# Kernel tuning notes

Measured on AMD Instinct MI355X. Metric: run time of the kernel, lower is better.

Reference implementation:

```python
import jax, jax.numpy as jnp
import numpy as np

S = 4096          # num tokens
H = 2304          # hidden_size
NQ = 8            # num query heads
NKV = 4           # num kv heads
HD = 256          # head_dim
INTER = 9216      # intermediate_size
SOFTCAP = 50.0    # attn_logit_softcapping
WINDOW = 1024     # sliding window
EPS = 1e-6
THETA = 10000.0
SCALE = 256.0 ** -0.5  # query_pre_attn_scalar ** -0.5


def rmsnorm(x, w, eps=EPS):
    # GemmaRMSNorm: x / rms(x) * (1 + w)
    var = jnp.mean(x * x, axis=-1, keepdims=True)
    return x * jax.lax.rsqrt(var + eps) * (1.0 + w)


def apply_rope(x, positions):
    # x: [S, nh, HD], neox style (rotate halves)
    half = HD // 2
    inv_freq = 1.0 / (THETA ** (jnp.arange(0, half, dtype=jnp.float32) / half))
    freqs = positions.astype(jnp.float32)[:, None] * inv_freq[None, :]  # [S, half]
    cos = jnp.cos(freqs)[:, None, :]
    sin = jnp.sin(freqs)[:, None, :]
    x1, x2 = x[..., :half], x[..., half:]
    return jnp.concatenate([x1 * cos - x2 * sin, x2 * cos + x1 * sin], axis=-1)


def setup_inputs() -> dict:
    key = jax.random.key(0)
    ks = jax.random.split(key, 6)
    w_std = 0.02
    return {
        "positions": jnp.arange(S, dtype=jnp.int32),
        "hidden_states": jax.random.normal(ks[0], (S, H), dtype=jnp.float32),
        "w_qkv": jax.random.normal(ks[1], (H, (NQ + 2 * NKV) * HD), dtype=jnp.float32) * w_std,
        "w_o": jax.random.normal(ks[2], (NQ * HD, H), dtype=jnp.float32) * w_std,
        "w_gate_up": jax.random.normal(ks[3], (H, 2 * INTER), dtype=jnp.float32) * w_std,
        "w_down": jax.random.normal(ks[4], (INTER, H), dtype=jnp.float32) * w_std,
        "w_in_ln": jnp.zeros((H,), jnp.float32),
        "w_post_attn_ln": jnp.zeros((H,), jnp.float32),
        "w_pre_ff_ln": jnp.zeros((H,), jnp.float32),
        "w_post_ff_ln": jnp.zeros((H,), jnp.float32),
    }


def attention(positions, h, w_qkv, w_o):
    qkv = h @ w_qkv  # [S, (NQ+2*NKV)*HD]
    q, k, v = jnp.split(qkv, [NQ * HD, (NQ + NKV) * HD], axis=-1)
    q = q.reshape(S, NQ, HD)
    k = k.reshape(S, NKV, HD)
    v = v.reshape(S, NKV, HD)
    q = apply_rope(q, positions)
    k = apply_rope(k, positions)
    # GQA: repeat kv heads
    rep = NQ // NKV
    k = jnp.repeat(k, rep, axis=1)  # [S, NQ, HD]
    v = jnp.repeat(v, rep, axis=1)
    scores = jnp.einsum("qhd,khd->hqk", q, k) * SCALE  # [NQ, S, S]
    # Gemma2 logit soft-capping
    scores = SOFTCAP * jnp.tanh(scores / SOFTCAP)
    # causal + sliding window mask
    i = jnp.arange(S)[:, None]
    j = jnp.arange(S)[None, :]
    ok = (j <= i) & (i - j < WINDOW)
    scores = jnp.where(ok[None], scores, -jnp.inf)
    probs = jax.nn.softmax(scores, axis=-1)
    out = jnp.einsum("hqk,khd->qhd", probs, v).reshape(S, NQ * HD)
    return out @ w_o


def mlp(x, w_gate_up, w_down):
    gu = x @ w_gate_up  # [S, 2*INTER]
    gate, up = jnp.split(gu, 2, axis=-1)
    return (jax.nn.gelu(gate, approximate=True) * up) @ w_down


def reference(positions, hidden_states, w_qkv, w_o, w_gate_up, w_down,
              w_in_ln, w_post_attn_ln, w_pre_ff_ln, w_post_ff_ln):
    # residual is None on entry (first layer semantics)
    residual = hidden_states
    h = rmsnorm(hidden_states, w_in_ln)
    h = attention(positions, h, w_qkv, w_o)
    h = rmsnorm(h, w_post_attn_ln)
    # fused add + norm: residual <- h + residual ; h <- norm(residual)
    residual = h + residual
    h = rmsnorm(residual, w_pre_ff_ln)
    h = mlp(h, w_gate_up, w_down)
    h = rmsnorm(h, w_post_ff_ln)
    return (h, residual)
```

## Files before the change

### kernel.cpp

```cpp
#include <hip/hip_runtime.h>
#include <cstdint>
#include <cmath>

#define S_LEN 4096
#define H_DIM 2304
#define NQH   8
#define NKVH  4
#define HDIM  256
#define INTER 9216
#define QKV_N 4096
#define QH    2048
#define KVH   1024

typedef __attribute__((ext_vector_type(4))) float  f32x4;
typedef __attribute__((ext_vector_type(8))) __bf16 bf16x8;

__device__ __forceinline__ __bf16 f2bf(float f) {
  union { float f; unsigned u; } x; x.f = f;
  unsigned r = (x.u + 0x7fffu + ((x.u >> 16) & 1u)) >> 16;
  union { unsigned short s; __bf16 b; } y; y.s = (unsigned short)r;
  return y.b;
}

__device__ __forceinline__ void g2l16(const void* g, void* l) {
  __builtin_amdgcn_global_load_lds(
      (__attribute__((address_space(1))) void*)(uintptr_t)g,
      (__attribute__((address_space(3))) void*)(uint32_t)(uintptr_t)l, 16, 0, 0);
}

__device__ __forceinline__ float block_sum(float v, float* sbuf) {
  #pragma unroll
  for (int o = 32; o > 0; o >>= 1) v += __shfl_xor(v, o);
  __syncthreads();
  if ((threadIdx.x & 63) == 0) sbuf[threadIdx.x >> 6] = v;
  __syncthreads();
  return sbuf[0] + sbuf[1] + sbuf[2] + sbuf[3];
}

__global__ void conv_t64(const float* __restrict__ src, __bf16* __restrict__ dst,
                         int srcStride, int dstStride) {
  __shared__ float t[64 * 65];
  int tid = threadIdx.x;
  long n0 = (long)blockIdx.x * 64, k0 = (long)blockIdx.y * 64;
  int tx = tid & 15;
  int ky = tid >> 4;
  #pragma unroll
  for (int l = 0; l < 4; ++l) {
    int k = ky + l * 16;
    f32x4 v = *(const f32x4*)(src + (k0 + k) * srcStride + n0 + tx * 4);
    #pragma unroll
    for (int e = 0; e < 4; ++e) t[(tx * 4 + e) * 65 + k] = v[e];
  }
  __syncthreads();
  int ny = tid >> 2, kc = (tid & 3) * 16;
  bf16x8 a, b;
  #pragma unroll
  for (int i = 0; i < 8; ++i) a[i] = f2bf(t[ny * 65 + kc + i]);
  #pragma unroll
  for (int i = 0; i < 8; ++i) b[i] = f2bf(t[ny * 65 + kc + 8 + i]);
  __bf16* d = dst + (n0 + ny) * dstStride + k0 + kc;
  *(bf16x8*)d = a;
  *(bf16x8*)(d + 8) = b;
}

__device__ __forceinline__ int gu_map(int n) {
  int t = n >> 7, w = (n >> 6) & 1, j = (n >> 4) & 3, c = n & 15;
  int a = t * 64 + w * 32 + ((j >> 1) << 4) + c;
  return (j & 1) ? (INTER + a) : a;
}

__global__ void conv_gu64(const float* __restrict__ src, __bf16* __restrict__ dst) {
  __shared__ float t[64 * 65];
  int tid = threadIdx.x;
  long n0 = (long)blockIdx.x * 64, k0 = (long)blockIdx.y * 64;
  int tx = tid & 15, ky = tid >> 4;
  int sc = gu_map((int)n0 + tx * 4);
  #pragma unroll
  for (int l = 0; l < 4; ++l) {
    int k = ky + l * 16;
    f32x4 v = *(const f32x4*)(src + (k0 + k) * (2 * INTER) + sc);
    #pragma unroll
    for (int e = 0; e < 4; ++e) t[(tx * 4 + e) * 65 + k] = v[e];
  }
  __syncthreads();
  int ny = tid >> 2, kc = (tid & 3) * 16;
  bf16x8 a, b;
  #pragma unroll
  for (int i = 0; i < 8; ++i) a[i] = f2bf(t[ny * 65 + kc + i]);
  #pragma unroll
  for (int i = 0; i < 8; ++i) b[i] = f2bf(t[ny * 65 + kc + 8 + i]);
  __bf16* d = dst + (n0 + ny) * H_DIM + k0 + kc;
  *(bf16x8*)d = a;
  *(bf16x8*)(d + 8) = b;
}

__global__ void rms_in_kernel(const float* __restrict__ x, const float* __restrict__ w,
                              __bf16* __restrict__ out) {
  __shared__ float sbuf[4];
  int row = blockIdx.x, tid = threadIdx.x;
  const float* xr = x + (long)row * H_DIM;
  float v[9]; float ss = 0.f;
  #pragma unroll
  for (int i = 0; i < 9; ++i) { v[i] = xr[tid + i * 256]; ss += v[i] * v[i]; }
  ss = block_sum(ss, sbuf);
  float inv = rsqrtf(ss * (1.0f / H_DIM) + 1e-6f);
  #pragma unroll
  for (int i = 0; i < 9; ++i)
    out[(long)row * H_DIM + tid + i * 256] = f2bf(v[i] * inv * (1.f + w[tid + i * 256]));
}

__global__ void rms_post_attn_kernel(const float* __restrict__ P, const float* __restrict__ hidden,
                                     const float* __restrict__ w_post, const float* __restrict__ w_pre,
                                     float* __restrict__ resid, __bf16* __restrict__ x2) {
  __shared__ float sbuf[4];
  int row = blockIdx.x, tid = threadIdx.x;
  const float* pr = P + (long)row * H_DIM;
  const float* hr = hidden + (long)row * H_DIM;
  float pv[9]; float ss = 0.f;
  #pragma unroll
  for (int i = 0; i < 9; ++i) { pv[i] = pr[tid + i * 256]; ss += pv[i] * pv[i]; }
  ss = block_sum(ss, sbuf);
  float inv = rsqrtf(ss * (1.0f / H_DIM) + 1e-6f);
  float rv[9]; float ss2 = 0.f;
  #pragma unroll
  for (int i = 0; i < 9; ++i) {
    int c = tid + i * 256;
    float hn = pv[i] * inv * (1.f + w_post[c]);
    rv[i] = hn + hr[c];
    resid[(long)row * H_DIM + c] = rv[i];
    ss2 += rv[i] * rv[i];
  }
  ss2 = block_sum(ss2, sbuf);
  float inv2 = rsqrtf(ss2 * (1.0f / H_DIM) + 1e-6f);
  #pragma unroll
  for (int i = 0; i < 9; ++i) {
    int c = tid + i * 256;
    x2[(long)row * H_DIM + c] = f2bf(rv[i] * inv2 * (1.f + w_pre[c]));
  }
}

__global__ void rms_final_kernel(const float* __restrict__ x, const float* __restrict__ w,
                                 float* __restrict__ out) {
  __shared__ float sbuf[4];
  int row = blockIdx.x, tid = threadIdx.x;
  const float* xr = x + (long)row * H_DIM;
  float v[9]; float ss = 0.f;
  #pragma unroll
  for (int i = 0; i < 9; ++i) { v[i] = xr[tid + i * 256]; ss += v[i] * v[i]; }
  ss = block_sum(ss, sbuf);
  float inv = rsqrtf(ss * (1.0f / H_DIM) + 1e-6f);
  #pragma unroll
  for (int i = 0; i < 9; ++i)
    out[(long)row * H_DIM + tid + i * 256] = v[i] * inv * (1.f + w[tid + i * 256]);
}

__global__ void rope_kernel(const float* __restrict__ qkv, const int* __restrict__ positions,
                            __bf16* __restrict__ Qr, __bf16* __restrict__ Kr) {
  int row = blockIdx.x, tid = threadIdx.x;
  float pos = (float)positions[row];
  const float LOG_TH_128 = 9.210340371976184f / 128.f;
  bool isQ = tid < 128;
  int c = isQ ? tid : (tid - 128);
  int hh = c >> 4;
  int d0 = (c & 15) * 8;
  const float* base = qkv + (long)row * QKV_N + (isQ ? 0 : QH) + hh * 256;
  f32x4 x1a = *(const f32x4*)(base + d0);
  f32x4 x1b = *(const f32x4*)(base + d0 + 4);
  f32x4 x2a = *(const f32x4*)(base + d0 + 128);
  f32x4 x2b = *(const f32x4*)(base + d0 + 132);
  bf16x8 lo, hi;
  #pragma unroll
  for (int j = 0; j < 8; ++j) {
    float x1 = j < 4 ? x1a[j] : x1b[j - 4];
    float x2 = j < 4 ? x2a[j] : x2b[j - 4];
    float fr = pos * expf(-(float)(d0 + j) * LOG_TH_128);
    float sn, cs; sincosf(fr, &sn, &cs);
    lo[j] = f2bf(x1 * cs - x2 * sn);
    hi[j] = f2bf(x2 * cs + x1 * sn);
  }
  __bf16* out = (isQ ? Qr + (long)row * QH : Kr + (long)row * KVH) + hh * 256;
  *(bf16x8*)(out + d0) = lo;
  *(bf16x8*)(out + 128 + d0) = hi;
}

template <int EPI>
__global__ void gemm_bt(const __bf16* __restrict__ A, const __bf16* __restrict__ B,
                        void* __restrict__ Cout, int K, int ldc) {
  __shared__ __bf16 As[128 * 64];
  __shared__ __bf16 Bs[128 * 64];
  int tid = threadIdx.x;
  int wave = tid >> 6, lane = tid & 63;
  int wm = wave >> 1, wn = wave & 1;
  int q4 = lane >> 4, l15 = lane & 15;

  int nwgx = gridDim.x;
  int nwg = nwgx * gridDim.y;
  int orig = blockIdx.y * nwgx + blockIdx.x;
  int qd = nwg >> 3, rm = nwg & 7;
  int xcd = orig & 7, idx = orig >> 3;
  int swz = (xcd < rm ? xcd * (qd + 1) : rm * (qd + 1) + (xcd - rm) * qd) + idx;
  long bm = (long)(swz / nwgx) * 128, bn = (long)(swz % nwgx) * 128;

  int r8 = tid >> 3;
  int cs = (tid & 7) ^ (r8 & 7);
  const __bf16* Ag = A + (bm + r8) * K + cs * 8;
  const __bf16* Bg = B + (bn + r8) * K + cs * 8;
  __bf16* Asd = As + tid * 8;
  __bf16* Bsd = Bs + tid * 8;

  int moff[4], noff[4];
  #pragma unroll
  for (int i = 0; i < 4; ++i) {
    moff[i] = (wm * 64 + i * 16 + l15) * 64;
    noff[i] = (wn * 64 + i * 16 + l15) * 64;
  }
  int c0 = (q4 ^ (l15 & 7)) * 8;
  f32x4 acc[4][4] = {};

  for (int k0 = 0; k0 < K; k0 += 64) {
    #pragma unroll
    for (int l = 0; l < 4; ++l) {
      g2l16(Ag + (long)(l * 32) * K, Asd + l * 2048);
      g2l16(Bg + (long)(l * 32) * K, Bsd + l * 2048);
    }
    Ag += 64; Bg += 64;
    __syncthreads();
    #pragma unroll
    for (int ks = 0; ks < 2; ++ks) {
      int cc = c0 ^ (ks * 32);
      bf16x8 af[4], bfv[4];
      #pragma unroll
      for (int i = 0; i < 4; ++i) af[i]  = *(const bf16x8*)(As + moff[i] + cc);
      #pragma unroll
      for (int j = 0; j < 4; ++j) bfv[j] = *(const bf16x8*)(Bs + noff[j] + cc);
      #pragma unroll
      for (int i = 0; i < 4; ++i)
        #pragma unroll
        for (int j = 0; j < 4; ++j)
          acc[i][j] = __builtin_amdgcn_mfma_f32_16x16x32_bf16(af[i], bfv[j], acc[i][j], 0, 0, 0);
    }
    __syncthreads();
  }

  if (EPI == 0) {
    float* C = (float*)Cout;
    #pragma unroll
    for (int i = 0; i < 4; ++i)
      #pragma unroll
      for (int r = 0; r < 4; ++r) {
        long m = bm + wm * 64 + i * 16 + q4 * 4 + r;
        #pragma unroll
        for (int j = 0; j < 4; ++j)
          C[m * ldc + bn + wn * 64 + j * 16 + l15] = acc[i][j][r];
      }
  } else {
    __bf16* C = (__bf16*)Cout;
    #pragma unroll
    for (int i = 0; i < 4; ++i)
      #pragma unroll
      for (int r = 0; r < 4; ++r) {
        long m = bm + wm * 64 + i * 16 + q4 * 4 + r;
        #pragma unroll
        for (int jj = 0; jj < 2; ++jj) {
          float gt = acc[i][2 * jj][r];
          float up = acc[i][2 * jj + 1][r];
          float u = 0.7978845608f * (gt + 0.044715f * gt * gt * gt);
          float e = __builtin_amdgcn_exp2f(u * 2.8853900817779268f);
          float gl = gt * (1.0f - __builtin_amdgcn_rcpf(e + 1.0f));
          long a = (bn >> 1) + wn * 32 + jj * 16 + l15;
          C[m * ldc + a] = f2bf(gl * up);
        }
      }
  }
}

template <int EPI>
__global__ __launch_bounds__(512, 2)
void gemm8(const __bf16* __restrict__ A, const __bf16* __restrict__ B,
           void* __restrict__ Cout, int K, int ldc) {
  __shared__ __bf16 As[2][16384];
  __shared__ __bf16 Bs[2][16384];
  const __bf16* Asb = (const __bf16*)As;
  const __bf16* Bsb = (const __bf16*)Bs;

  int tid = threadIdx.x;
  int wave = tid >> 6, lane = tid & 63;
  int wm = wave >> 2;
  int wn = wave & 3;
  int q4 = lane >> 4, l15 = lane & 15;
  int xk = l15 & 7;

  int nwgx = gridDim.x;
  int nwg = nwgx * gridDim.y;
  int orig = blockIdx.y * nwgx + blockIdx.x;
  int qd = nwg >> 3, rm = nwg & 7;
  int xcd = orig & 7, idx = orig >> 3;
  int swz = (xcd < rm ? xcd * (qd + 1) : rm * (qd + 1) + (xcd - rm) * qd) + idx;
  long bm = (long)(swz / nwgx) * 256;
  long bn = (long)(swz % nwgx) * 256;

  int rr = tid >> 3;
  int cs = (tid & 7) ^ (rr & 7);
  const __bf16* Ag = A + (bm + rr) * (long)K + cs * 8;
  const __bf16* Bg = B + (bn + rr) * (long)K + cs * 8;
  __bf16* Asd = (__bf16*)As + tid * 8;
  __bf16* Bsd = (__bf16*)Bs + tid * 8;

#define ST_A(buf, h, kof) do { \
    g2l16(Ag + ((h) * 128LL      ) * K + (kof), Asd + (buf) * 16384 + (h) * 8192); \
    g2l16(Ag + ((h) * 128LL + 64 ) * K + (kof), Asd + (buf) * 16384 + (h) * 8192 + 4096); } while (0)
#define ST_B(buf, h, kof) do { \
    g2l16(Bg + ((h) * 128LL      ) * K + (kof), Bsd + (buf) * 16384 + (h) * 8192); \
    g2l16(Bg + ((h) * 128LL + 64 ) * K + (kof), Bsd + (buf) * 16384 + (h) * 8192 + 4096); } while (0)

  int aOff[4], bOff[4];
  #pragma unroll
  for (int i = 0; i < 4; ++i) {
    aOff[i] = (wm * 64 + i * 16 + l15) * 64;
    bOff[i] = (wn * 64 + i * 16 + l15) * 64;
  }

#define PH_LOAD_A(buf, mh, ks) \
  { _Pragma("unroll") for (int f = 0; f < 4; ++f) \
      afr[f] = *(const bf16x8*)(Asb + (buf) * 16384 + (mh) * 8192 + aOff[f] + ((((ks) * 4 + q4) ^ xk) * 8)); }
#define PH_LOAD_B(buf) \
  { _Pragma("unroll") for (int ks2 = 0; ks2 < 2; ++ks2) \
    _Pragma("unroll") for (int j = 0; j < 4; ++j) \
      bfr[ks2][j] = *(const bf16x8*)(Bsb + (buf) * 16384 + bOff[j] + (((ks2 * 4 + q4) ^ xk) * 8)); }
#define PH_CORE(mh, ks) \
  __builtin_amdgcn_s_barrier(); \
  asm volatile("s_waitcnt lgkmcnt(0)" ::: "memory"); \
  __builtin_amdgcn_s_setprio(1); \
  { _Pragma("unroll") for (int f = 0; f < 4; ++f) \
    _Pragma("unroll") for (int j = 0; j < 4; ++j) \
      acc[(mh) * 4 + f][j] = __builtin_amdgcn_mfma_f32_16x16x32_bf16(afr[f], bfr[ks][j], acc[(mh) * 4 + f][j], 0, 0, 0); } \
  __builtin_amdgcn_s_setprio(0)
#define BAR   __builtin_amdgcn_s_barrier()
#define WVM6  asm volatile("s_waitcnt vmcnt(6)" ::: "memory")
#define WVM0  asm volatile("s_waitcnt vmcnt(0)" ::: "memory")

  f32x4 acc[8][4] = {};
  bf16x8 bfr[2][4];
  bf16x8 afr[4];

  int nt = K >> 6;
  int nit = (nt >> 1) - 1;

  ST_B(0, 0, 0); ST_B(0, 1, 0); ST_A(0, 0, 0); ST_A(0, 1, 0);
  ST_B(1, 0, 64); ST_B(1, 1, 64); ST_A(1, 0, 64);
  WVM6;
  BAR;

  for (int it = 0; it < nit; ++it) {
    const long k0 = (long)it * 128;
    PH_LOAD_B(0); PH_LOAD_A(0, 0, 0); ST_A(1, 1, k0 + 64);
    asm volatile("s_waitcnt lgkmcnt(8)" ::: "memory");
    PH_CORE(0, 0); BAR;
    PH_LOAD_A(0, 0, 1); ST_B(0, 0, k0 + 128);
    PH_CORE(0, 1); BAR;
    PH_LOAD_A(0, 1, 0); ST_B(0, 1, k0 + 128);
    PH_CORE(1, 0); BAR;
    PH_LOAD_A(0, 1, 1); ST_A(0, 0, k0 + 128);
    PH_CORE(1, 1); WVM6; BAR;
    PH_LOAD_B(1); PH_LOAD_A(1, 0, 0); ST_A(0, 1, k0 + 128);
    asm volatile("s_waitcnt lgkmcnt(8)" ::: "memory");
    PH_CORE(0, 0); BAR;
    PH_LOAD_A(1, 0, 1); ST_B(1, 0, k0 + 192);
    PH_CORE(0, 1); BAR;
    PH_LOAD_A(1, 1, 0); ST_B(1, 1, k0 + 192);
    PH_CORE(1, 0); BAR;
    PH_LOAD_A(1, 1, 1); ST_A(1, 0, k0 + 192);
    PH_CORE(1, 1); WVM6; BAR;
  }

  {
    const long k0 = (long)(nt - 2) * 64;
    PH_LOAD_B(0); PH_LOAD_A(0, 0, 0); ST_A(1, 1, k0 + 64);
    asm volatile("s_waitcnt lgkmcnt(8)" ::: "memory");
    PH_CORE(0, 0); BAR;
    PH_LOAD_A(0, 0, 1); PH_CORE(0, 1); BAR;
    PH_LOAD_A(0, 1, 0); PH_CORE(1, 0); BAR;
    PH_LOAD_A(0, 1, 1); PH_CORE(1, 1); WVM0; BAR;
    PH_LOAD_B(1); PH_LOAD_A(1, 0, 0); PH_CORE(0, 0); BAR;
    PH_LOAD_A(1, 0, 1); PH_CORE(0, 1); BAR;
    PH_LOAD_A(1, 1, 0); PH_CORE(1, 0); BAR;
    PH_LOAD_A(1, 1, 1); PH_CORE(1, 1);
  }

#undef ST_A
#undef ST_B
#undef PH_LOAD_A
#undef PH_LOAD_B
#undef PH_CORE
#undef BAR
#undef WVM6
#undef WVM0

  if (EPI == 0) {
    float* C = (float*)Cout;
    #pragma unroll
    for (int mi = 0; mi < 8; ++mi) {
      int mh = mi >> 2, f = mi & 3;
      #pragma unroll
      for (int r = 0; r < 4; ++r) {
        long m = bm + mh * 128 + wm * 64 + f * 16 + q4 * 4 + r;
        #pragma unroll
        for (int j = 0; j < 4; ++j)
          C[m * ldc + bn + wn * 64 + j * 16 + l15] = acc[mi][j][r];
      }
    }
  } else {
    __bf16* C = (__bf16*)Cout;
    #pragma unroll
    for (int mi = 0; mi < 8; ++mi) {
      int mh = mi >> 2, f = mi & 3;
      #pragma unroll
      for (int r = 0; r < 4; ++r) {
        long m = bm + mh * 128 + wm * 64 + f * 16 + q4 * 4 + r;
        #pragma unroll
        for (int jj = 0; jj < 2; ++jj) {
          float gt = acc[mi][2 * jj][r];
          float up = acc[mi][2 * jj + 1][r];
          float u = 0.7978845608f * (gt + 0.044715f * gt * gt * gt);
          float e = __builtin_amdgcn_exp2f(u * 2.8853900817779268f);
          float gl = gt * (1.0f - __builtin_amdgcn_rcpf(e + 1.0f));
          long a = (bn >> 1) + (wn >> 1) * 64 + (wn & 1) * 32 + jj * 16 + l15;
          C[m * ldc + a] = f2bf(gl * up);
        }
      }
    }
  }
}

__global__ void attn_kernel(const __bf16* __restrict__ Qr, const __bf16* __restrict__ Kr,
                            const __bf16* __restrict__ VT, __bf16* __restrict__ AT) {
  __shared__ __bf16 Kt[64 * 256];
  __shared__ __bf16 Vt[256 * 64];
  __shared__ __bf16 Pt[4][16 * 72];
  int tid = threadIdx.x, wave = tid >> 6, lane = tid & 63;
  int q4 = lane >> 4, l15 = lane & 15;
  int h = blockIdx.y, hk = h >> 1;
  int qb = blockIdx.x * 64;
  int wqb = qb + wave * 16;

  bf16x8 qf[8];
  {
    const __bf16* qp = Qr + (long)(wqb + l15) * QH + h * HDIM + q4 * 8;
    #pragma unroll
    for (int ks = 0; ks < 8; ++ks) qf[ks] = *(const bf16x8*)(qp + ks * 32);
  }
  f32x4 Oa[16] = {};
  float lsum[4] = {0.f, 0.f, 0.f, 0.f};

  int csk = (tid & 31) ^ ((tid >> 5) & 7);
  const __bf16* Kh = Kr + (long)(tid >> 5) * KVH + hk * HDIM + csk * 8;
  int csv = (tid & 7) ^ ((tid >> 3) & 7);
  const __bf16* Vh = VT + (long)(hk * HDIM + (tid >> 3)) * S_LEN + csv * 8;

  int lo = qb - 1023; if (lo < 0) lo = 0;
  int t0 = lo >> 6, t1 = qb >> 6;
  for (int t = t0; t <= t1; ++t) {
    int k0 = t * 64;
    #pragma unroll
    for (int l = 0; l < 8; ++l) {
      g2l16(Kh + ((long)k0 + l * 8) * KVH, Kt + tid * 8 + l * 2048);
      g2l16(Vh + k0 + (long)(l * 32) * S_LEN, Vt + tid * 8 + l * 2048);
    }
    __syncthreads();
    bool active = (k0 <= wqb + 15) && (k0 + 63 >= wqb - 1023);
    if (active) {
      f32x4 Sa[4] = {};
      #pragma unroll
      for (int ks = 0; ks < 8; ++ks)
        #pragma unroll
        for (int j = 0; j < 4; ++j) {
          int key = j * 16 + l15;
          int cc = (ks * 4 + q4) ^ (l15 & 7);
          bf16x8 kf = *(const bf16x8*)(Kt + key * 256 + cc * 8);
          Sa[j] = __builtin_amdgcn_mfma_f32_16x16x32_bf16(qf[ks], kf, Sa[j], 0, 0, 0);
        }
      #pragma unroll
      for (int r = 0; r < 4; ++r) {
        int qi = wqb + q4 * 4 + r;
        #pragma unroll
        for (int j = 0; j < 4; ++j) {
          int kj = k0 + j * 16 + l15;
          float y = Sa[j][r] * 1.25e-3f;
          float e = __builtin_amdgcn_exp2f(y * 2.8853900817779268f);
          float p = __builtin_amdgcn_exp2f(72.13475204444817f
                     - 144.26950408889634f * __builtin_amdgcn_rcpf(e + 1.0f));
          bool ok = (kj <= qi) && (qi - kj < 1024);
          p = ok ? p : 0.0f;
          lsum[r] += p;
          Pt[wave][(q4 * 4 + r) * 72 + j * 16 + l15] = f2bf(p);
        }
      }
      asm volatile("s_waitcnt lgkmcnt(0)" ::: "memory");
      bf16x8 pf[2];
      #pragma unroll
      for (int ks = 0; ks < 2; ++ks)
        pf[ks] = *(const bf16x8*)(&Pt[wave][l15 * 72 + ks * 32 + q4 * 8]);
      #pragma unroll
      for (int f = 0; f < 16; ++f) {
        int d = f * 16 + l15;
        #pragma unroll
        for (int ks = 0; ks < 2; ++ks) {
          int cc = (ks * 4 + q4) ^ (l15 & 7);
          bf16x8 vf = *(const bf16x8*)(Vt + d * 64 + cc * 8);
          Oa[f] = __builtin_amdgcn_mfma_f32_16x16x32_bf16(pf[ks], vf, Oa[f], 0, 0, 0);
        }
      }
    }
    __syncthreads();
  }
  #pragma unroll
  for (int r = 0; r < 4; ++r) {
    float v = lsum[r];
    #pragma unroll
    for (int o = 1; o < 16; o <<= 1) v += __shfl_xor(v, o);
    lsum[r] = __builtin_amdgcn_rcpf(v);
  }
  #pragma unroll
  for (int f = 0; f < 16; ++f)
    #pragma unroll
    for (int r = 0; r < 4; ++r) {
      long qi = wqb + q4 * 4 + r;
      AT[qi * QH + h * HDIM + f * 16 + l15] = f2bf(Oa[f][r] * lsum[r]);
    }
}

extern "C" void kernel_launch(void* const* d_in, const int* in_sizes, int n_in,
                              void* d_out, int out_size, void* d_ws, size_t ws_size,
                              hipStream_t stream) {
  (void)in_sizes; (void)n_in; (void)out_size; (void)ws_size;
  const int*   positions = (const int*)d_in[0];
  const float* hidden    = (const float*)d_in[1];
  const float* w_qkv     = (const float*)d_in[2];
  const float* w_o       = (const float*)d_in[3];
  const float* w_gu      = (const float*)d_in[4];
  const float* w_dn      = (const float*)d_in[5];
  const float* w_in_ln   = (const float*)d_in[6];
  const float* w_post    = (const float*)d_in[7];
  const float* w_pre     = (const float*)d_in[8];
  const float* w_pff     = (const float*)d_in[9];
  float* out_h   = (float*)d_out;
  float* out_res = out_h + (size_t)S_LEN * H_DIM;

  char* p = (char*)d_ws;
  auto take = [&](size_t b) { char* r = p; p += (b + 255) & ~(size_t)255; return r; };
  __bf16* Wqkv = (__bf16*)take((size_t)QKV_N * H_DIM * 2);
  __bf16* Wo   = (__bf16*)take((size_t)H_DIM * QH * 2);
  __bf16* Wgu  = (__bf16*)take((size_t)2 * INTER * H_DIM * 2);
  __bf16* Wdn  = (__bf16*)take((size_t)H_DIM * INTER * 2);
  __bf16* Xn   = (__bf16*)take((size_t)S_LEN * H_DIM * 2);
  char*   Rbig = take((size_t)S_LEN * INTER * 2);
  __bf16* Qrb  = (__bf16*)take((size_t)S_LEN * QH * 2);
  __bf16* Krb  = (__bf16*)take((size_t)S_LEN * KVH * 2);
  __bf16* VTb  = (__bf16*)take((size_t)KVH * S_LEN * 2);
  __bf16* ATb  = (__bf16*)take((size_t)S_LEN * QH * 2);
  float*  Pf   = (float*)take((size_t)S_LEN * H_DIM * 4);
  __bf16* X2   = (__bf16*)take((size_t)S_LEN * H_DIM * 2);
  float*  QKV  = (float*)Rbig;
  __bf16* ACT  = (__bf16*)Rbig;
  float*  Mbuf = Pf;

  dim3 blk(256);
  conv_t64<<<dim3(QKV_N / 64, H_DIM / 64), blk, 0, stream>>>(w_qkv, Wqkv, QKV_N, H_DIM);
  conv_t64<<<dim3(H_DIM / 64, QH / 64),    blk, 0, stream>>>(w_o,   Wo,   H_DIM, QH);
  conv_gu64<<<dim3(2 * INTER / 64, H_DIM / 64), blk, 0, stream>>>(w_gu, Wgu);
  conv_t64<<<dim3(H_DIM / 64, INTER / 64), blk, 0, stream>>>(w_dn,  Wdn,  H_DIM, INTER);
  rms_in_kernel<<<S_LEN, blk, 0, stream>>>(hidden, w_in_ln, Xn);
  gemm8<0><<<dim3(QKV_N / 256, S_LEN / 256), dim3(512), 0, stream>>>(Xn, Wqkv, QKV, H_DIM, QKV_N);
  rope_kernel<<<S_LEN, dim3(192), 0, stream>>>(QKV, positions, Qrb, Krb);
  conv_t64<<<dim3(KVH / 64, S_LEN / 64), blk, 0, stream>>>(QKV + QH + KVH, VTb, QKV_N, S_LEN);
  attn_kernel<<<dim3(S_LEN / 64, NQH), blk, 0, stream>>>(Qrb, Krb, VTb, ATb);
  gemm_bt<0><<<dim3(H_DIM / 128, S_LEN / 128), blk, 0, stream>>>(ATb, Wo, Pf, QH, H_DIM);
  rms_post_attn_kernel<<<S_LEN, blk, 0, stream>>>(Pf, hidden, w_post, w_pre, out_res, X2);
  gemm8<1><<<dim3(2 * INTER / 256, S_LEN / 256), dim3(512), 0, stream>>>(X2, Wgu, ACT, H_DIM, INTER);
  gemm_bt<0><<<dim3(H_DIM / 128, S_LEN / 128), blk, 0, stream>>>(ACT, Wdn, Mbuf, INTER, H_DIM);
  rms_final_kernel<<<S_LEN, blk, 0, stream>>>(Mbuf, w_pff, out_h);
}
```

Baseline: 1.237 ms.

## Fuse RoPE and V transpose into QKV GEMM epilogue; double-buffer attention K/V

The QKV GEMM gains a third epilogue that applies RoPE to Q/K tiles through shared memory and writes V transposed in bf16. This removes the fp32 QKV intermediate, the separate rope kernel and the V transpose kernel. The attention kernel now uses 512 threads over 128-query blocks and double-buffers its K/V tiles in LDS so loads for the next tile overlap compute. The larger LDS footprint of attention (launch bounds of one block) may lower occupancy, and the RoPE epilogue adds barriers and sincos work inside the GEMM.

```diff
diff --git a/kernel.cpp b/kernel.cpp
--- a/kernel.cpp
+++ b/kernel.cpp
@@ -14,6 +14,7 @@
 
 typedef __attribute__((ext_vector_type(4))) float  f32x4;
 typedef __attribute__((ext_vector_type(8))) __bf16 bf16x8;
+typedef __attribute__((ext_vector_type(4))) __bf16 bf16x4;
 
 __device__ __forceinline__ __bf16 f2bf(float f) {
   union { float f; unsigned u; } x; x.f = f;
@@ -152,35 +153,6 @@
   #pragma unroll
   for (int i = 0; i < 9; ++i)
     out[(long)row * H_DIM + tid + i * 256] = v[i] * inv * (1.f + w[tid + i * 256]);
-}
-
-__global__ void rope_kernel(const float* __restrict__ qkv, const int* __restrict__ positions,
-                            __bf16* __restrict__ Qr, __bf16* __restrict__ Kr) {
-  int row = blockIdx.x, tid = threadIdx.x;
-  float pos = (float)positions[row];
-  const float LOG_TH_128 = 9.210340371976184f / 128.f;
-  bool isQ = tid < 128;
-  int c = isQ ? tid : (tid - 128);
-  int hh = c >> 4;
-  int d0 = (c & 15) * 8;
-  const float* base = qkv + (long)row * QKV_N + (isQ ? 0 : QH) + hh * 256;
-  f32x4 x1a = *(const f32x4*)(base + d0);
-  f32x4 x1b = *(const f32x4*)(base + d0 + 4);
-  f32x4 x2a = *(const f32x4*)(base + d0 + 128);
-  f32x4 x2b = *(const f32x4*)(base + d0 + 132);
-  bf16x8 lo, hi;
-  #pragma unroll
-  for (int j = 0; j < 8; ++j) {
-    float x1 = j < 4 ? x1a[j] : x1b[j - 4];
-    float x2 = j < 4 ? x2a[j] : x2b[j - 4];
-    float fr = pos * expf(-(float)(d0 + j) * LOG_TH_128);
-    float sn, cs; sincosf(fr, &sn, &cs);
-    lo[j] = f2bf(x1 * cs - x2 * sn);
-    hi[j] = f2bf(x2 * cs + x1 * sn);
-  }
-  __bf16* out = (isQ ? Qr + (long)row * QH : Kr + (long)row * KVH) + hh * 256;
-  *(bf16x8*)(out + d0) = lo;
-  *(bf16x8*)(out + 128 + d0) = hi;
 }
 
 template <int EPI>
@@ -277,11 +249,15 @@
 template <int EPI>
 __global__ __launch_bounds__(512, 2)
 void gemm8(const __bf16* __restrict__ A, const __bf16* __restrict__ B,
-           void* __restrict__ Cout, int K, int ldc) {
-  __shared__ __bf16 As[2][16384];
-  __shared__ __bf16 Bs[2][16384];
-  const __bf16* Asb = (const __bf16*)As;
-  const __bf16* Bsb = (const __bf16*)Bs;
+           void* __restrict__ Cout, int K, int ldc,
+           const int* __restrict__ positions,
+           __bf16* __restrict__ QrO, __bf16* __restrict__ KrO,
+           __bf16* __restrict__ VTO) {
+  __shared__ __bf16 smemb[65536];
+  __bf16* Asmem = smemb;
+  __bf16* Bsmem = smemb + 32768;
+  const __bf16* Asb = Asmem;
+  const __bf16* Bsb = Bsmem;
 
   int tid = threadIdx.x;
   int wave = tid >> 6, lane = tid & 63;
@@ -303,8 +279,8 @@
   int cs = (tid & 7) ^ (rr & 7);
   const __bf16* Ag = A + (bm + rr) * (long)K + cs * 8;
   const __bf16* Bg = B + (bn + rr) * (long)K + cs * 8;
-  __bf16* Asd = (__bf16*)As + tid * 8;
-  __bf16* Bsd = (__bf16*)Bs + tid * 8;
+  __bf16* Asd = Asmem + tid * 8;
+  __bf16* Bsd = Bsmem + tid * 8;
 
 #define ST_A(buf, h, kof) do { \
     g2l16(Ag + ((h) * 128LL      ) * K + (kof), Asd + (buf) * 16384 + (h) * 8192); \
@@ -409,7 +385,7 @@
           C[m * ldc + bn + wn * 64 + j * 16 + l15] = acc[mi][j][r];
       }
     }
-  } else {
+  } else if (EPI == 1) {
     __bf16* C = (__bf16*)Cout;
     #pragma unroll
     for (int mi = 0; mi < 8; ++mi) {
@@ -429,18 +405,84 @@
         }
       }
     }
-  }
-}
-
-__global__ void attn_kernel(const __bf16* __restrict__ Qr, const __bf16* __restrict__ Kr,
-                            const __bf16* __restrict__ VT, __bf16* __restrict__ AT) {
-  __shared__ __bf16 Kt[64 * 256];
-  __shared__ __bf16 Vt[256 * 64];
-  __shared__ __bf16 Pt[4][16 * 72];
+  } else {
+    int nb = (int)(bn >> 8);
+    if (nb >= 12) {
+      int hv = nb - 12;
+      #pragma unroll
+      for (int mi = 0; mi < 8; ++mi) {
+        int mh = mi >> 2, f = mi & 3;
+        long m0 = bm + mh * 128 + wm * 64 + f * 16 + q4 * 4;
+        #pragma unroll
+        for (int j = 0; j < 4; ++j) {
+          int c = wn * 64 + j * 16 + l15;
+          bf16x4 pk;
+          #pragma unroll
+          for (int r = 0; r < 4; ++r) pk[r] = f2bf(acc[mi][j][r]);
+          *(bf16x4*)(VTO + (long)(hv * 256 + c) * S_LEN + m0) = pk;
+        }
+      }
+    } else {
+      float* Lf = (float*)smemb;
+      bool isQ = nb < 8;
+      __bf16* Op = isQ ? QrO : KrO;
+      long rstride = isQ ? QH : KVH;
+      int hh = isQ ? nb : nb - 8;
+      const float LOG_TH_128 = 0.07195578415294675f;
+      #pragma unroll
+      for (int mh = 0; mh < 2; ++mh) {
+        __syncthreads();
+        if (wn >= 2) {
+          #pragma unroll
+          for (int f = 0; f < 4; ++f) {
+            int row = wm * 64 + f * 16 + q4 * 4;
+            #pragma unroll
+            for (int j = 0; j < 4; ++j) {
+              int d = (wn - 2) * 64 + j * 16 + l15;
+              #pragma unroll
+              for (int r = 0; r < 4; ++r)
+                Lf[(row + r) * 132 + d] = acc[mh * 4 + f][j][r];
+            }
+          }
+        }
+        __syncthreads();
+        if (wn < 2) {
+          #pragma unroll
+          for (int f = 0; f < 4; ++f) {
+            #pragma unroll
+            for (int r = 0; r < 4; ++r) {
+              int rl = wm * 64 + f * 16 + q4 * 4 + r;
+              long m = bm + mh * 128 + rl;
+              float pos = (float)positions[m];
+              #pragma unroll
+              for (int j = 0; j < 4; ++j) {
+                int d = wn * 64 + j * 16 + l15;
+                float x1 = acc[mh * 4 + f][j][r];
+                float x2 = Lf[rl * 132 + d];
+                float fr = pos * expf(-(float)d * LOG_TH_128);
+                float sn, cc; sincosf(fr, &sn, &cc);
+                __bf16* op = Op + m * rstride + hh * 256 + d;
+                op[0]   = f2bf(x1 * cc - x2 * sn);
+                op[128] = f2bf(x2 * cc + x1 * sn);
+              }
+            }
+          }
+        }
+      }
+    }
+  }
+}
+
+__global__ __launch_bounds__(512, 1)
+void attn_kernel(const __bf16* __restrict__ Qr, const __bf16* __restrict__ Kr,
+                 const __bf16* __restrict__ VT, __bf16* __restrict__ AT) {
+  __shared__ __bf16 Kt[2][64 * 256];
+  __shared__ __bf16 Vt[2][256 * 64];
+  __shared__ __bf16 Pt[8][16 * 72];
   int tid = threadIdx.x, wave = tid >> 6, lane = tid & 63;
   int q4 = lane >> 4, l15 = lane & 15;
   int h = blockIdx.y, hk = h >> 1;
-  int qb = blockIdx.x * 64;
+  int qb = blockIdx.x * 128;
   int wqb = qb + wave * 16;
 
   bf16x8 qf[8];
@@ -458,15 +500,30 @@
   const __bf16* Vh = VT + (long)(hk * HDIM + (tid >> 3)) * S_LEN + csv * 8;
 
   int lo = qb - 1023; if (lo < 0) lo = 0;
-  int t0 = lo >> 6, t1 = qb >> 6;
+  int t0 = lo >> 6, t1 = (qb + 127) >> 6;
+
+#define STAGE(t, b) do { \
+    int k0s = (t) * 64; \
+    _Pragma("unroll") \
+    for (int l = 0; l < 4; ++l) { \
+      g2l16(Kh + ((long)k0s + l * 16) * KVH, &Kt[(b)][tid * 8 + l * 4096]); \
+      g2l16(Vh + k0s + (long)(l * 64) * S_LEN, &Vt[(b)][tid * 8 + l * 4096]); \
+    } } while (0)
+
+  STAGE(t0, 0);
+  asm volatile("s_waitcnt vmcnt(0)" ::: "memory");
+  __builtin_amdgcn_s_barrier();
+
   for (int t = t0; t <= t1; ++t) {
+    int b = (t - t0) & 1;
+    if (t < t1) {
+      STAGE(t + 1, b ^ 1);
+      asm volatile("s_waitcnt vmcnt(8)" ::: "memory");
+    } else {
+      asm volatile("s_waitcnt vmcnt(0)" ::: "memory");
+    }
+    __builtin_amdgcn_s_barrier();
     int k0 = t * 64;
-    #pragma unroll
-    for (int l = 0; l < 8; ++l) {
-      g2l16(Kh + ((long)k0 + l * 8) * KVH, Kt + tid * 8 + l * 2048);
-      g2l16(Vh + k0 + (long)(l * 32) * S_LEN, Vt + tid * 8 + l * 2048);
-    }
-    __syncthreads();
     bool active = (k0 <= wqb + 15) && (k0 + 63 >= wqb - 1023);
     if (active) {
       f32x4 Sa[4] = {};
@@ -476,7 +533,7 @@
         for (int j = 0; j < 4; ++j) {
           int key = j * 16 + l15;
           int cc = (ks * 4 + q4) ^ (l15 & 7);
-          bf16x8 kf = *(const bf16x8*)(Kt + key * 256 + cc * 8);
+          bf16x8 kf = *(const bf16x8*)(&Kt[b][key * 256 + cc * 8]);
           Sa[j] = __builtin_amdgcn_mfma_f32_16x16x32_bf16(qf[ks], kf, Sa[j], 0, 0, 0);
         }
       #pragma unroll
@@ -506,13 +563,15 @@
         #pragma unroll
         for (int ks = 0; ks < 2; ++ks) {
           int cc = (ks * 4 + q4) ^ (l15 & 7);
-          bf16x8 vf = *(const bf16x8*)(Vt + d * 64 + cc * 8);
+          bf16x8 vf = *(const bf16x8*)(&Vt[b][d * 64 + cc * 8]);
           Oa[f] = __builtin_amdgcn_mfma_f32_16x16x32_bf16(pf[ks], vf, Oa[f], 0, 0, 0);
         }
       }
     }
-    __syncthreads();
-  }
+    __builtin_amdgcn_s_barrier();
+  }
+#undef STAGE
+
   #pragma unroll
   for (int r = 0; r < 4; ++r) {
     float v = lsum[r];
@@ -560,7 +619,6 @@
   __bf16* ATb  = (__bf16*)take((size_t)S_LEN * QH * 2);
   float*  Pf   = (float*)take((size_t)S_LEN * H_DIM * 4);
   __bf16* X2   = (__bf16*)take((size_t)S_LEN * H_DIM * 2);
-  float*  QKV  = (float*)Rbig;
   __bf16* ACT  = (__bf16*)Rbig;
   float*  Mbuf = Pf;
 
@@ -570,13 +628,13 @@
   conv_gu64<<<dim3(2 * INTER / 64, H_DIM / 64), blk, 0, stream>>>(w_gu, Wgu);
   conv_t64<<<dim3(H_DIM / 64, INTER / 64), blk, 0, stream>>>(w_dn,  Wdn,  H_DIM, INTER);
   rms_in_kernel<<<S_LEN, blk, 0, stream>>>(hidden, w_in_ln, Xn);
-  gemm8<0><<<dim3(QKV_N / 256, S_LEN / 256), dim3(512), 0, stream>>>(Xn, Wqkv, QKV, H_DIM, QKV_N);
-  rope_kernel<<<S_LEN, dim3(192), 0, stream>>>(QKV, positions, Qrb, Krb);
-  conv_t64<<<dim3(KVH / 64, S_LEN / 64), blk, 0, stream>>>(QKV + QH + KVH, VTb, QKV_N, S_LEN);
-  attn_kernel<<<dim3(S_LEN / 64, NQH), blk, 0, stream>>>(Qrb, Krb, VTb, ATb);
+  gemm8<2><<<dim3(QKV_N / 256, S_LEN / 256), dim3(512), 0, stream>>>(
+      Xn, Wqkv, nullptr, H_DIM, QKV_N, positions, Qrb, Krb, VTb);
+  attn_kernel<<<dim3(S_LEN / 128, NQH), dim3(512), 0, stream>>>(Qrb, Krb, VTb, ATb);
   gemm_bt<0><<<dim3(H_DIM / 128, S_LEN / 128), blk, 0, stream>>>(ATb, Wo, Pf, QH, H_DIM);
   rms_post_attn_kernel<<<S_LEN, blk, 0, stream>>>(Pf, hidden, w_post, w_pre, out_res, X2);
-  gemm8<1><<<dim3(2 * INTER / 256, S_LEN / 256), dim3(512), 0, stream>>>(X2, Wgu, ACT, H_DIM, INTER);
+  gemm8<1><<<dim3(2 * INTER / 256, S_LEN / 256), dim3(512), 0, stream>>>(
+      X2, Wgu, ACT, H_DIM, INTER, nullptr, nullptr, nullptr, nullptr);
   gemm_bt<0><<<dim3(H_DIM / 128, S_LEN / 128), blk, 0, stream>>>(ACT, Wdn, Mbuf, INTER, H_DIM);
   rms_final_kernel<<<S_LEN, blk, 0, stream>>>(Mbuf, w_pff, out_h);
 }
```

New measurement: 1.315 ms. +6.3%, slower.

## Double-buffer K/V tiles in attention and widen blocks to 128 queries

Applied to the files above, without the earlier changes.

The attention kernel now covers 128 query rows per block with 512 threads instead of 64 rows with 256 threads. This halves the number of times each K/V tile is staged into LDS per query. K and V tiles are double-buffered in LDS, and the next tile's async loads are issued before computing on the current one, with vmcnt waits and raw s_barrier replacing __syncthreads. The cost is a larger LDS footprint and a launch bound of one block per CU. The grid shrinks to 256 blocks, which lowers occupancy and gives coarser load balance across the sliding-window range.

```diff
diff --git a/kernel.cpp b/kernel.cpp
--- a/kernel.cpp
+++ b/kernel.cpp
@@ -432,15 +432,16 @@
   }
 }
 
-__global__ void attn_kernel(const __bf16* __restrict__ Qr, const __bf16* __restrict__ Kr,
-                            const __bf16* __restrict__ VT, __bf16* __restrict__ AT) {
-  __shared__ __bf16 Kt[64 * 256];
-  __shared__ __bf16 Vt[256 * 64];
-  __shared__ __bf16 Pt[4][16 * 72];
+__global__ __launch_bounds__(512, 1)
+void attn_kernel(const __bf16* __restrict__ Qr, const __bf16* __restrict__ Kr,
+                 const __bf16* __restrict__ VT, __bf16* __restrict__ AT) {
+  __shared__ __bf16 Kt[2][64 * 256];
+  __shared__ __bf16 Vt[2][256 * 64];
+  __shared__ __bf16 Pt[8][16 * 72];
   int tid = threadIdx.x, wave = tid >> 6, lane = tid & 63;
   int q4 = lane >> 4, l15 = lane & 15;
   int h = blockIdx.y, hk = h >> 1;
-  int qb = blockIdx.x * 64;
+  int qb = blockIdx.x * 128;
   int wqb = qb + wave * 16;
 
   bf16x8 qf[8];
@@ -458,15 +459,30 @@
   const __bf16* Vh = VT + (long)(hk * HDIM + (tid >> 3)) * S_LEN + csv * 8;
 
   int lo = qb - 1023; if (lo < 0) lo = 0;
-  int t0 = lo >> 6, t1 = qb >> 6;
+  int t0 = lo >> 6, t1 = (qb + 127) >> 6;
+
+#define STAGE(t, b) do { \
+    int k0s = (t) * 64; \
+    _Pragma("unroll") \
+    for (int l = 0; l < 4; ++l) { \
+      g2l16(Kh + ((long)k0s + l * 16) * KVH, &Kt[(b)][tid * 8 + l * 4096]); \
+      g2l16(Vh + k0s + (long)(l * 64) * S_LEN, &Vt[(b)][tid * 8 + l * 4096]); \
+    } } while (0)
+
+  STAGE(t0, 0);
+  asm volatile("s_waitcnt vmcnt(0)" ::: "memory");
+  __builtin_amdgcn_s_barrier();
+
   for (int t = t0; t <= t1; ++t) {
+    int b = (t - t0) & 1;
+    if (t < t1) {
+      STAGE(t + 1, b ^ 1);
+      asm volatile("s_waitcnt vmcnt(8)" ::: "memory");
+    } else {
+      asm volatile("s_waitcnt vmcnt(0)" ::: "memory");
+    }
+    __builtin_amdgcn_s_barrier();
     int k0 = t * 64;
-    #pragma unroll
-    for (int l = 0; l < 8; ++l) {
-      g2l16(Kh + ((long)k0 + l * 8) * KVH, Kt + tid * 8 + l * 2048);
-      g2l16(Vh + k0 + (long)(l * 32) * S_LEN, Vt + tid * 8 + l * 2048);
-    }
-    __syncthreads();
     bool active = (k0 <= wqb + 15) && (k0 + 63 >= wqb - 1023);
     if (active) {
       f32x4 Sa[4] = {};
@@ -476,7 +492,7 @@
         for (int j = 0; j < 4; ++j) {
           int key = j * 16 + l15;
           int cc = (ks * 4 + q4) ^ (l15 & 7);
-          bf16x8 kf = *(const bf16x8*)(Kt + key * 256 + cc * 8);
+          bf16x8 kf = *(const bf16x8*)(&Kt[b][key * 256 + cc * 8]);
           Sa[j] = __builtin_amdgcn_mfma_f32_16x16x32_bf16(qf[ks], kf, Sa[j], 0, 0, 0);
         }
       #pragma unroll
@@ -506,13 +522,15 @@
         #pragma unroll
         for (int ks = 0; ks < 2; ++ks) {
           int cc = (ks * 4 + q4) ^ (l15 & 7);
-          bf16x8 vf = *(const bf16x8*)(Vt + d * 64 + cc * 8);
+          bf16x8 vf = *(const bf16x8*)(&Vt[b][d * 64 + cc * 8]);
           Oa[f] = __builtin_amdgcn_mfma_f32_16x16x32_bf16(pf[ks], vf, Oa[f], 0, 0, 0);
         }
       }
     }
-    __syncthreads();
-  }
+    __builtin_amdgcn_s_barrier();
+  }
+#undef STAGE
+
   #pragma unroll
   for (int r = 0; r < 4; ++r) {
     float v = lsum[r];
@@ -573,7 +591,7 @@
   gemm8<0><<<dim3(QKV_N / 256, S_LEN / 256), dim3(512), 0, stream>>>(Xn, Wqkv, QKV, H_DIM, QKV_N);
   rope_kernel<<<S_LEN, dim3(192), 0, stream>>>(QKV, positions, Qrb, Krb);
   conv_t64<<<dim3(KVH / 64, S_LEN / 64), blk, 0, stream>>>(QKV + QH + KVH, VTb, QKV_N, S_LEN);
-  attn_kernel<<<dim3(S_LEN / 64, NQH), blk, 0, stream>>>(Qrb, Krb, VTb, ATb);
+  attn_kernel<<<dim3(S_LEN / 128, NQH), dim3(512), 0, stream>>>(Qrb, Krb, VTb, ATb);
   gemm_bt<0><<<dim3(H_DIM / 128, S_LEN / 128), blk, 0, stream>>>(ATb, Wo, Pf, QH, H_DIM);
   rms_post_attn_kernel<<<S_LEN, blk, 0, stream>>>(Pf, hidden, w_post, w_pre, out_res, X2);
   gemm8<1><<<dim3(2 * INTER / 256, S_LEN / 256), dim3(512), 0, stream>>>(X2, Wgu, ACT, H_DIM, INTER);
```

After: 1.181 ms. 1.05x faster.
